# Kernel optimization log

Hardware: AMD Instinct MI355X
Metric: run time of the kernel (lower is better)

## Reference

```python
import jax, jax.numpy as jnp
import numpy as np

B, C, N, T = 8, 256, 768, 12
HID = C // 4          # divided_hidden=4 -> hidden=64
HEADS = 1
D = HID // HEADS      # head_dim = 64
SCALE = D ** (-0.5)
EPS = 1e-6


def conv1x1(x, w, b):
    # x: [b,c,n,t], w: [o,c], b: [o]
    return jnp.einsum('bcnt,oc->bont', x, w) + b[:, None, None]


def layernorm_cf(x, w, b):
    # channels_first LayerNorm over axis 1
    u = x.mean(1, keepdims=True)
    s = ((x - u) ** 2).mean(1, keepdims=True)
    xh = (x - u) / jnp.sqrt(s + EPS)
    return w[:, None, None] * xh + b[:, None, None]


def setup_inputs() -> dict:
    key = jax.random.key(0)
    ks = jax.random.split(key, 32)
    f32 = jnp.float32
    inp = {
        'x': jax.random.normal(ks[0], (B, C, N, T), dtype=f32),
        'time_ind': jax.random.randint(ks[1], (B, T), 0, 288),
        'weekin': jax.random.randint(ks[2], (B, T), 0, 7),
        'holiin': jax.random.randint(ks[3], (B, T), 0, 2),
        'adj_s': jax.random.uniform(ks[4], (B, T, N, N), dtype=f32),
        'ln1_w': jnp.ones((C,), f32), 'ln1_b': jnp.zeros((C,), f32),
        'ln2_w': jnp.ones((C,), f32), 'ln2_b': jnp.zeros((C,), f32),
        'Wnq': jax.random.normal(ks[5], (C, HID), f32) * 0.05, 'bnq': jnp.zeros((HID,), f32),
        'Wnk': jax.random.normal(ks[6], (C, HID), f32) * 0.05, 'bnk': jnp.zeros((HID,), f32),
        'Wtq': jax.random.normal(ks[7], (C, HID), f32) * 0.05, 'btq': jnp.zeros((HID,), f32),
        'Wtk': jax.random.normal(ks[8], (C, HID), f32) * 0.05, 'btk': jnp.zeros((HID,), f32),
        'Bn': jax.random.normal(ks[9], (1, HEADS, N, N), f32) * 0.02,
        'Bt': jax.random.normal(ks[10], (1, HEADS, T, T), f32) * 0.02,
        'v_w': jax.random.normal(ks[11], (HID, C), f32) * 0.05, 'v_b': jnp.zeros((HID,), f32),
        'fcv_w': jax.random.normal(ks[12], (2 * HID, C), f32) * 0.05, 'fcv_b': jnp.zeros((2 * HID,), f32),
        'proj_w': jax.random.normal(ks[13], (C, 2 * HID), f32) * 0.05, 'proj_b': jnp.zeros((C,), f32),
        'ffn_w1': jax.random.normal(ks[14], (4 * C, C), f32) * 0.03, 'ffn_b1': jnp.zeros((4 * C,), f32),
        'ffn_w2': jax.random.normal(ks[15], (C, 2 * C), f32) * 0.03, 'ffn_b2': jnp.zeros((C,), f32),
    }
    return inp


def dual_axis(x, adj_s, Wnq, bnq, Wnk, bnk, Wtq, btq, Wtk, btk, Bn, Bt,
              v_w, v_b, fcv_w, fcv_b, proj_w, proj_b):
    # x: [b,f,n,t]; heads==1 so head dim folds into hidden.
    # --- node-axis attention ---
    xn = x.transpose(0, 3, 2, 1)                      # [b,t,n,f]
    nq = xn @ Wnq + bnq                               # [b,t,n,hid]
    nk = xn @ Wnk + bnk
    attn_n = jnp.einsum('btid,btjd->btij', nq, nk) * SCALE + Bn[0, 0]
    attn_n = jax.nn.softmax(attn_n, axis=-1) * adj_s  # [b,t,n,n]
    # --- time-axis attention ---
    xt = x.transpose(0, 2, 3, 1)                      # [b,n,t,f]
    tq = xt @ Wtq + btq                               # [b,n,t,hid]
    tk = xt @ Wtk + btk
    attn_t = jnp.einsum('bnid,bnjd->bnij', tq, tk) * SCALE + Bt[0, 0]
    attn_t = jax.nn.softmax(attn_t, axis=-1)          # [b,n,t,t]
    # --- values + nconv_2 aggregation ---
    v1 = conv1x1(x, v_w, v_b)                         # [b,hid,n,t]
    # sg: out[b,c,w,l] = sum_v v1[b,c,v,l] * attn_n[b,l,v,w]
    hs = jnp.einsum('bcvl,blvw->bcwl', v1, attn_n)    # [b,hid,n,t]
    # tg on time axis: v1 transposed to [b,hid,t,n]
    xtv = v1.transpose(0, 1, 3, 2)                    # [b,hid,t,n]
    tx = jnp.einsum('bcvl,blvw->bcwl', xtv, attn_t)   # [b,hid,t,n]
    ht = tx.transpose(0, 1, 3, 2)                     # [b,hid,n,t]
    h = jnp.concatenate([ht, hs], axis=1)             # [b,2hid,n,t]
    v = conv1x1(x, fcv_w, fcv_b)                      # [b,2hid,n,t]
    return conv1x1(h * v, proj_w, proj_b)             # [b,C,n,t]


def feedforward(x, w1, b1, w2, b2):
    y = conv1x1(x, w1, b1)                            # [b,4C,n,t]
    a, g = jnp.split(y, 2, axis=1)                    # each [b,2C,n,t]
    y = a * jax.nn.gelu(g, approximate=False)
    return conv1x1(y, w2, b2)


def reference(x, time_ind, weekin, holiin, adj_s,
              ln1_w, ln1_b, ln2_w, ln2_b,
              Wnq, bnq, Wnk, bnk, Wtq, btq, Wtk, btk, Bn, Bt,
              v_w, v_b, fcv_w, fcv_b, proj_w, proj_b,
              ffn_w1, ffn_b1, ffn_w2, ffn_b2):
    x1 = layernorm_cf(x, ln1_w, ln1_b)
    x = dual_axis(x1, adj_s, Wnq, bnq, Wnk, bnk, Wtq, btq, Wtk, btk, Bn, Bt,
                  v_w, v_b, fcv_w, fcv_b, proj_w, proj_b) + x
    x2 = layernorm_cf(x, ln2_w, ln2_b)
    x = feedforward(x2, ffn_w1, ffn_b1, ffn_w2, ffn_b2) + x
    return x
```

## Files before the change

kernel.cpp:

```cpp
#include <hip/hip_runtime.h>
#include <cstddef>

typedef unsigned short u16;
typedef __attribute__((ext_vector_type(8))) short bf16x8;
typedef __attribute__((ext_vector_type(4))) float f32x4;

constexpr int nB = 8, nC = 256, nN = 768, nT = 12, nM = nN * nT, nH = 64;
constexpr float SCALE = 0.125f;
constexpr float LNEPS = 1e-6f;

__device__ inline u16 f2b(float f) {
    union { float f; unsigned u; } v; v.f = f;
    unsigned r = v.u + 0x7FFFu + ((v.u >> 16) & 1u);
    return (u16)(r >> 16);
}
__device__ inline float b2f(u16 h) {
    union { unsigned u; float f; } v; v.u = ((unsigned)h) << 16;
    return v.f;
}
__device__ inline uint2 packb4(float a, float b, float c, float d) {
    uint2 r;
    r.x = (unsigned)f2b(a) | ((unsigned)f2b(b) << 16);
    r.y = (unsigned)f2b(c) | ((unsigned)f2b(d) << 16);
    return r;
}
__device__ inline f32x4 mfma16(bf16x8 a, bf16x8 b, f32x4 c) {
    return __builtin_amdgcn_mfma_f32_16x16x32_bf16(a, b, c, 0, 0, 0);
}

__device__ inline void stage64(const u16* __restrict__ g, int ld, u16* lds, int tid) {
#pragma unroll
    for (int r = 0; r < 2; ++r) {
        int c = tid + r * 256;
        int row = c >> 3, kc = (c & 7) * 8;
        *(uint4*)&lds[row * 72 + kc] = *(const uint4*)&g[(size_t)row * ld + kc];
    }
}

__device__ inline void mfma_block(const u16* As, const u16* Bs, f32x4 acc[2][2],
                                  int wo, int wm, int quad, int r) {
#pragma unroll
    for (int ks = 0; ks < 64; ks += 32) {
        bf16x8 a0 = *(const bf16x8*)&As[(wo + r) * 72 + ks + quad * 8];
        bf16x8 a1 = *(const bf16x8*)&As[(wo + 16 + r) * 72 + ks + quad * 8];
        bf16x8 b0 = *(const bf16x8*)&Bs[(wm + r) * 72 + ks + quad * 8];
        bf16x8 b1 = *(const bf16x8*)&Bs[(wm + 16 + r) * 72 + ks + quad * 8];
        acc[0][0] = mfma16(a0, b0, acc[0][0]);
        acc[0][1] = mfma16(a0, b1, acc[0][1]);
        acc[1][0] = mfma16(a1, b0, acc[1][0]);
        acc[1][1] = mfma16(a1, b1, acc[1][1]);
    }
}

__global__ __launch_bounds__(256) void cvt_w(const float* __restrict__ Wnq,
                                             const float* __restrict__ Wnk,
                                             const float* __restrict__ Wtq,
                                             const float* __restrict__ Wtk,
                                             const float* __restrict__ vw,
                                             const float* __restrict__ fcvw,
                                             const float* __restrict__ projw,
                                             const float* __restrict__ w1,
                                             const float* __restrict__ w2,
                                             u16* __restrict__ WB) {
    int i = blockIdx.x * 256 + threadIdx.x;
    float v;
    if (i < 65536) {
        int seg = i >> 14, j = i & 16383;
        int o = j >> 8, k = j & 255;
        const float* src = seg == 0 ? Wnq : seg == 1 ? Wnk : seg == 2 ? Wtq : Wtk;
        v = src[k * 64 + o];
    } else if (i < 81920)  v = vw[i - 65536];
    else if (i < 114688)   v = fcvw[i - 81920];
    else if (i < 147456)   v = projw[i - 114688];
    else if (i < 409600)   v = w1[i - 147456];
    else                   v = w2[i - 409600];
    WB[i] = f2b(v);
}

__global__ __launch_bounds__(256) void zero_f(float* __restrict__ p) {
    p[blockIdx.x * 256 + threadIdx.x] = 0.f;
}

__global__ __launch_bounds__(256) void ln_cl(const float* __restrict__ X,
                                             const float* __restrict__ w,
                                             const float* __restrict__ bias,
                                             u16* __restrict__ Y) {
    int tid = threadIdx.x;
    int lane = tid & 63, cg = tid >> 6;
    int m0 = blockIdx.x * 64, b = blockIdx.y;
    size_t base = (size_t)b * nC * nM + m0 + lane;
    float s = 0.f, ss = 0.f;
#pragma unroll 4
    for (int k = 0; k < 64; ++k) {
        float v = X[base + (size_t)(cg * 64 + k) * nM];
        s += v; ss += v * v;
    }
    __shared__ float rs[4][64], rss[4][64], mu_s[64], rstd_s[64];
    __shared__ u16 Lo[64][264];
    rs[cg][lane] = s; rss[cg][lane] = ss;
    __syncthreads();
    if (tid < 64) {
        float t1 = rs[0][lane] + rs[1][lane] + rs[2][lane] + rs[3][lane];
        float t2 = rss[0][lane] + rss[1][lane] + rss[2][lane] + rss[3][lane];
        float mu = t1 * (1.f / nC);
        float var = t2 * (1.f / nC) - mu * mu;
        mu_s[lane] = mu;
        rstd_s[lane] = rsqrtf(var + LNEPS);
    }
    __syncthreads();
    float mu = mu_s[lane], rstd = rstd_s[lane];
#pragma unroll 8
    for (int k = 0; k < 64; k += 2) {
        int c = cg * 64 + k;
        float v0 = (X[base + (size_t)c * nM] - mu) * rstd * w[c] + bias[c];
        float v1 = (X[base + (size_t)(c + 1) * nM] - mu) * rstd * w[c + 1] + bias[c + 1];
        *(unsigned*)&Lo[lane][c] = (unsigned)f2b(v0) | ((unsigned)f2b(v1) << 16);
    }
    __syncthreads();
#pragma unroll
    for (int r = 0; r < 8; ++r) {
        int c = tid + r * 256;
        int mm = c >> 5, ch = (c & 31) * 8;
        *(uint4*)&Y[((size_t)b * nM + m0 + mm) * 256 + ch] = *(uint4*)&Lo[mm][ch];
    }
}

template <int COUT, int LAYOUT>
__global__ __launch_bounds__(256) void gemm_proj(const u16* __restrict__ X,
                                                 const u16* __restrict__ W,
                                                 const float* __restrict__ bias,
                                                 u16* __restrict__ OUT) {
    __shared__ u16 As[64 * 72], Bs[64 * 72];
    int tid = threadIdx.x;
    int m0 = blockIdx.x * 64, o0 = blockIdx.y * 64, b = blockIdx.z;
    int lane = tid & 63, wid = tid >> 6;
    int wo = (wid & 1) * 32, wm = (wid >> 1) * 32;
    int quad = lane >> 4, r = lane & 15;
    const u16* Ag = W + (size_t)o0 * 256;
    const u16* Bg = X + ((size_t)b * nM + m0) * 256;
    f32x4 acc[2][2] = {};
    for (int k0 = 0; k0 < 256; k0 += 64) {
        __syncthreads();
        stage64(Ag + k0, 256, As, tid);
        stage64(Bg + k0, 256, Bs, tid);
        __syncthreads();
        mfma_block(As, Bs, acc, wo, wm, quad, r);
    }
#pragma unroll
    for (int oi = 0; oi < 2; ++oi)
#pragma unroll
        for (int mj = 0; mj < 2; ++mj) {
            int o = o0 + wo + oi * 16 + quad * 4;
            int m = m0 + wm + mj * 16 + r;
            f32x4 a = acc[oi][mj];
            float v0 = a[0] + bias[o], v1 = a[1] + bias[o + 1];
            float v2 = a[2] + bias[o + 2], v3 = a[3] + bias[o + 3];
            if (LAYOUT == 1) {
                *(uint2*)&OUT[((size_t)b * nM + m) * COUT + o] = packb4(v0, v1, v2, v3);
            } else if (LAYOUT == 0) {
                int n = m / 12, t = m - n * 12;
                *(uint2*)&OUT[((size_t)(b * 12 + t) * nN + n) * COUT + o] =
                    packb4(v0, v1, v2, v3);
            } else {
                int n = m / 12, t = m - n * 12;
                size_t bt = (size_t)(b * 12 + t) * 64;
                OUT[(bt + o) * nN + n]     = f2b(v0);
                OUT[(bt + o + 1) * nN + n] = f2b(v1);
                OUT[(bt + o + 2) * nN + n] = f2b(v2);
                OUT[(bt + o + 3) * nN + n] = f2b(v3);
            }
        }
}

__global__ __launch_bounds__(256) void scores_k(const u16* __restrict__ NQ,
                                                const u16* __restrict__ NK,
                                                const float* __restrict__ Bn,
                                                u16* __restrict__ SE,
                                                float* __restrict__ rowsum) {
    __shared__ u16 As[64 * 72], Bs[64 * 72];
    __shared__ float lsum[64];
    int tid = threadIdx.x;
    int j0 = blockIdx.x * 64, i0 = blockIdx.y * 64, bt = blockIdx.z;
    if (tid < 64) lsum[tid] = 0.f;
    int lane = tid & 63, wid = tid >> 6;
    int wo = (wid & 1) * 32, wm = (wid >> 1) * 32;
    int quad = lane >> 4, r = lane & 15;
    const u16* Ag = NQ + ((size_t)bt * nN + i0) * 64;
    const u16* Bg = NK + ((size_t)bt * nN + j0) * 64;
    f32x4 acc[2][2] = {};
    __syncthreads();
    stage64(Ag, 64, As, tid);
    stage64(Bg, 64, Bs, tid);
    __syncthreads();
    mfma_block(As, Bs, acc, wo, wm, quad, r);
#pragma unroll
    for (int oi = 0; oi < 2; ++oi) {
        f32x4 rsm = {0.f, 0.f, 0.f, 0.f};
#pragma unroll
        for (int mj = 0; mj < 2; ++mj) {
            int i_ = i0 + wo + oi * 16 + quad * 4;
            int j_ = j0 + wm + mj * 16 + r;
#pragma unroll
            for (int rr = 0; rr < 4; ++rr) {
                float s = acc[oi][mj][rr] * SCALE + Bn[(size_t)(i_ + rr) * nN + j_];
                float e = expf(s);
                SE[((size_t)bt * nN + i_ + rr) * nN + j_] = f2b(e);
                rsm[rr] += e;
            }
        }
#pragma unroll
        for (int mask = 1; mask < 16; mask <<= 1) {
            rsm[0] += __shfl_xor(rsm[0], mask);
            rsm[1] += __shfl_xor(rsm[1], mask);
            rsm[2] += __shfl_xor(rsm[2], mask);
            rsm[3] += __shfl_xor(rsm[3], mask);
        }
        if (r == 0) {
#pragma unroll
            for (int rr = 0; rr < 4; ++rr)
                atomicAdd(&lsum[wo + oi * 16 + quad * 4 + rr], rsm[rr]);
        }
    }
    __syncthreads();
    if (tid < 64) atomicAdd(&rowsum[(size_t)bt * nN + i0 + tid], lsum[tid]);
}

__global__ __launch_bounds__(256) void attn_fin(const u16* __restrict__ SE,
                                                const float* __restrict__ adj,
                                                const float* __restrict__ rowsum,
                                                u16* __restrict__ AT2) {
    __shared__ u16 Ls[64 * 72];
    __shared__ float rinv[64];
    int tid = threadIdx.x;
    int w0 = blockIdx.x * 64, v0 = blockIdx.y * 64, bt = blockIdx.z;
    if (tid < 64) rinv[tid] = 1.f / rowsum[(size_t)bt * nN + v0 + tid];
    __syncthreads();
    {
        int v = tid >> 2, wc = (tid & 3) * 16;
        const u16* se = SE + ((size_t)bt * nN + v0 + v) * nN + w0 + wc;
        const float* ad = adj + ((size_t)bt * nN + v0 + v) * nN + w0 + wc;
        float ri = rinv[v];
        union { uint4 q; u16 s[8]; } p0, p1;
#pragma unroll
        for (int ii = 0; ii < 8; ++ii) p0.s[ii] = f2b(b2f(se[ii]) * ad[ii] * ri);
#pragma unroll
        for (int ii = 0; ii < 8; ++ii) p1.s[ii] = f2b(b2f(se[8 + ii]) * ad[8 + ii] * ri);
        *(uint4*)&Ls[v * 72 + wc] = p0.q;
        *(uint4*)&Ls[v * 72 + wc + 8] = p1.q;
    }
    __syncthreads();
    {
        int w = tid >> 2, vc = (tid & 3) * 16;
        union { uint4 q; u16 s[8]; } p0, p1;
#pragma unroll
        for (int ii = 0; ii < 8; ++ii) p0.s[ii] = Ls[(vc + ii) * 72 + w];
#pragma unroll
        for (int ii = 0; ii < 8; ++ii) p1.s[ii] = Ls[(vc + 8 + ii) * 72 + w];
        u16* op = AT2 + ((size_t)bt * nN + w0 + w) * nN + v0 + vc;
        *(uint4*)&op[0] = p0.q;
        *(uint4*)&op[8] = p1.q;
    }
}

__global__ __launch_bounds__(256) void node_agg_k(const u16* __restrict__ V1N,
                                                  const u16* __restrict__ AT2,
                                                  u16* __restrict__ HB) {
    __shared__ u16 As[64 * 72], Bs[64 * 72];
    int tid = threadIdx.x;
    int w0 = blockIdx.x * 64, bt = blockIdx.z;
    int b = bt / 12, l = bt - b * 12;
    int lane = tid & 63, wid = tid >> 6;
    int wo = (wid & 1) * 32, wm = (wid >> 1) * 32;
    int quad = lane >> 4, r = lane & 15;
    const u16* Ag = V1N + (size_t)bt * 64 * nN;
    const u16* Bg = AT2 + ((size_t)bt * nN + w0) * nN;
    f32x4 acc[2][2] = {};
    for (int k0 = 0; k0 < nN; k0 += 64) {
        __syncthreads();
        stage64(Ag + k0, nN, As, tid);
        stage64(Bg + k0, nN, Bs, tid);
        __syncthreads();
        mfma_block(As, Bs, acc, wo, wm, quad, r);
    }
#pragma unroll
    for (int oi = 0; oi < 2; ++oi)
#pragma unroll
        for (int mj = 0; mj < 2; ++mj) {
            int c = wo + oi * 16 + quad * 4;
            int w = w0 + wm + mj * 16 + r;
            f32x4 a = acc[oi][mj];
            *(uint2*)&HB[((size_t)b * nM + w * 12 + l) * 128 + 64 + c] =
                packb4(a[0], a[1], a[2], a[3]);
        }
}

__global__ __launch_bounds__(192) void time_attn(const u16* __restrict__ TQ,
                                                 const u16* __restrict__ TK,
                                                 const float* __restrict__ Bt,
                                                 float* __restrict__ AT) {
    int bn = blockIdx.x;
    __shared__ float tqs[nT * 64], tks[nT * 64], ss[nT * nT];
    __shared__ float inv_s[nT], max_s[nT];
    int tid = threadIdx.x;
    size_t base = (size_t)bn * nT * 64;
#pragma unroll
    for (int r = 0; r < 4; ++r) {
        int idx = tid + r * 192;
        tqs[idx] = b2f(TQ[base + idx]);
        tks[idx] = b2f(TK[base + idx]);
    }
    __syncthreads();
    if (tid < 144) {
        int i = tid / 12, j = tid % 12;
        float s = 0.f;
#pragma unroll
        for (int h = 0; h < 64; ++h) s += tqs[i * 64 + h] * tks[j * 64 + h];
        ss[tid] = s * SCALE + Bt[i * 12 + j];
    }
    __syncthreads();
    if (tid < 12) {
        float mx = -1e30f;
        for (int j = 0; j < 12; ++j) mx = fmaxf(mx, ss[tid * 12 + j]);
        float sm = 0.f;
        for (int j = 0; j < 12; ++j) sm += expf(ss[tid * 12 + j] - mx);
        max_s[tid] = mx; inv_s[tid] = 1.f / sm;
    }
    __syncthreads();
    if (tid < 144) {
        int i = tid / 12;
        AT[(size_t)bn * 144 + tid] = expf(ss[tid] - max_s[i]) * inv_s[i];
    }
}

__global__ __launch_bounds__(256) void time_agg_k(const u16* __restrict__ V1N,
                                                  const float* __restrict__ AT,
                                                  u16* __restrict__ HB) {
    int tid = threadIdx.x;
    int lane = tid & 63, cg = tid >> 6;
    int n = blockIdx.x * 64 + lane;
    int b = blockIdx.y;
    size_t bn = (size_t)b * nN + n;
#pragma unroll 2
    for (int cc = 0; cc < 16; ++cc) {
        int c = cg * 16 + cc;
        float acc[12] = {};
        for (int v = 0; v < 12; ++v) {
            float val = b2f(V1N[((size_t)(b * 12 + v) * 64 + c) * nN + n]);
            const float4* at4 = (const float4*)(AT + bn * 144 + v * 12);
            float4 a0 = at4[0], a1 = at4[1], a2 = at4[2];
            acc[0] += val * a0.x;  acc[1] += val * a0.y;
            acc[2] += val * a0.z;  acc[3] += val * a0.w;
            acc[4] += val * a1.x;  acc[5] += val * a1.y;
            acc[6] += val * a1.z;  acc[7] += val * a1.w;
            acc[8] += val * a2.x;  acc[9] += val * a2.y;
            acc[10] += val * a2.z; acc[11] += val * a2.w;
        }
#pragma unroll
        for (int t = 0; t < 12; ++t)
            HB[((size_t)b * nM + n * 12 + t) * 128 + c] = f2b(acc[t]);
    }
}

__global__ __launch_bounds__(256) void prodproj_k(const u16* __restrict__ HB,
                                                  const u16* __restrict__ VG,
                                                  const u16* __restrict__ W,
                                                  const float* __restrict__ bias,
                                                  const float* __restrict__ RES,
                                                  float* __restrict__ OUT) {
    __shared__ u16 As[64 * 72], Bs[64 * 72];
    int tid = threadIdx.x;
    int m0 = blockIdx.x * 64, o0 = blockIdx.y * 64, b = blockIdx.z;
    int lane = tid & 63, wid = tid >> 6;
    int wo = (wid & 1) * 32, wm = (wid >> 1) * 32;
    int quad = lane >> 4, r = lane & 15;
    f32x4 acc[2][2] = {};
    for (int k0 = 0; k0 < 128; k0 += 64) {
        __syncthreads();
        stage64(W + (size_t)o0 * 128 + k0, 128, As, tid);
#pragma unroll
        for (int rr = 0; rr < 2; ++rr) {
            int c = tid + rr * 256;
            int row = c >> 3, kc = (c & 7) * 8;
            size_t gi = ((size_t)b * nM + m0 + row) * 128 + k0 + kc;
            uint4 hv = *(const uint4*)&HB[gi];
            uint4 vv = *(const uint4*)&VG[gi];
            u16* hs = (u16*)&hv; u16* vs = (u16*)&vv;
            union { uint4 q; u16 s[8]; } ov;
#pragma unroll
            for (int q2 = 0; q2 < 8; ++q2) ov.s[q2] = f2b(b2f(hs[q2]) * b2f(vs[q2]));
            *(uint4*)&Bs[row * 72 + kc] = ov.q;
        }
        __syncthreads();
        mfma_block(As, Bs, acc, wo, wm, quad, r);
    }
#pragma unroll
    for (int oi = 0; oi < 2; ++oi)
#pragma unroll
        for (int mj = 0; mj < 2; ++mj) {
            int o = o0 + wo + oi * 16 + quad * 4;
            int m = m0 + wm + mj * 16 + r;
            f32x4 a = acc[oi][mj];
#pragma unroll
            for (int rr = 0; rr < 4; ++rr) {
                size_t idx = ((size_t)(b * nC + o + rr)) * nM + m;
                OUT[idx] = a[rr] + bias[o + rr] + RES[idx];
            }
        }
}

__global__ __launch_bounds__(256) void ffn1_k(const u16* __restrict__ X,
                                              const u16* __restrict__ W1,
                                              const float* __restrict__ B1,
                                              u16* __restrict__ G1) {
    __shared__ u16 As[64 * 72], Gs[64 * 72], Bs[64 * 72];
    int tid = threadIdx.x;
    int m0 = blockIdx.x * 64, o0 = blockIdx.y * 64, b = blockIdx.z;
    int lane = tid & 63, wid = tid >> 6;
    int wo = (wid & 1) * 32, wm = (wid >> 1) * 32;
    int quad = lane >> 4, r = lane & 15;
    f32x4 acca[2][2] = {}, accg[2][2] = {};
    for (int k0 = 0; k0 < 256; k0 += 64) {
        __syncthreads();
        stage64(W1 + (size_t)o0 * 256 + k0, 256, As, tid);
        stage64(W1 + (size_t)(512 + o0) * 256 + k0, 256, Gs, tid);
        stage64(X + ((size_t)b * nM + m0) * 256 + k0, 256, Bs, tid);
        __syncthreads();
#pragma unroll
        for (int ks = 0; ks < 64; ks += 32) {
            bf16x8 a0 = *(const bf16x8*)&As[(wo + r) * 72 + ks + quad * 8];
            bf16x8 a1 = *(const bf16x8*)&As[(wo + 16 + r) * 72 + ks + quad * 8];
            bf16x8 g0 = *(const bf16x8*)&Gs[(wo + r) * 72 + ks + quad * 8];
            bf16x8 g1 = *(const bf16x8*)&Gs[(wo + 16 + r) * 72 + ks + quad * 8];
            bf16x8 b0 = *(const bf16x8*)&Bs[(wm + r) * 72 + ks + quad * 8];
            bf16x8 b1 = *(const bf16x8*)&Bs[(wm + 16 + r) * 72 + ks + quad * 8];
            acca[0][0] = mfma16(a0, b0, acca[0][0]);
            acca[0][1] = mfma16(a0, b1, acca[0][1]);
            acca[1][0] = mfma16(a1, b0, acca[1][0]);
            acca[1][1] = mfma16(a1, b1, acca[1][1]);
            accg[0][0] = mfma16(g0, b0, accg[0][0]);
            accg[0][1] = mfma16(g0, b1, accg[0][1]);
            accg[1][0] = mfma16(g1, b0, accg[1][0]);
            accg[1][1] = mfma16(g1, b1, accg[1][1]);
        }
    }
#pragma unroll
    for (int oi = 0; oi < 2; ++oi)
#pragma unroll
        for (int mj = 0; mj < 2; ++mj) {
            int o = o0 + wo + oi * 16 + quad * 4;
            int m = m0 + wm + mj * 16 + r;
            float vals[4];
#pragma unroll
            for (int rr = 0; rr < 4; ++rr) {
                float aa = acca[oi][mj][rr] + B1[o + rr];
                float gg = accg[oi][mj][rr] + B1[512 + o + rr];
                float gl = 0.5f * gg * (1.f + erff(gg * 0.70710678118654752f));
                vals[rr] = aa * gl;
            }
            *(uint2*)&G1[((size_t)b * nM + m) * 512 + o] =
                packb4(vals[0], vals[1], vals[2], vals[3]);
        }
}

__global__ __launch_bounds__(256) void ffn2_k(const u16* __restrict__ G1,
                                              const u16* __restrict__ W2,
                                              const float* __restrict__ B2,
                                              const float* __restrict__ RES,
                                              float* __restrict__ OUT) {
    __shared__ u16 As[64 * 72], Bs[64 * 72];
    int tid = threadIdx.x;
    int m0 = blockIdx.x * 64, o0 = blockIdx.y * 64, b = blockIdx.z;
    int lane = tid & 63, wid = tid >> 6;
    int wo = (wid & 1) * 32, wm = (wid >> 1) * 32;
    int quad = lane >> 4, r = lane & 15;
    f32x4 acc[2][2] = {};
    for (int k0 = 0; k0 < 512; k0 += 64) {
        __syncthreads();
        stage64(W2 + (size_t)o0 * 512 + k0, 512, As, tid);
        stage64(G1 + ((size_t)b * nM + m0) * 512 + k0, 512, Bs, tid);
        __syncthreads();
        mfma_block(As, Bs, acc, wo, wm, quad, r);
    }
#pragma unroll
    for (int oi = 0; oi < 2; ++oi)
#pragma unroll
        for (int mj = 0; mj < 2; ++mj) {
            int o = o0 + wo + oi * 16 + quad * 4;
            int m = m0 + wm + mj * 16 + r;
            f32x4 a = acc[oi][mj];
#pragma unroll
            for (int rr = 0; rr < 4; ++rr) {
                size_t idx = ((size_t)(b * nC + o + rr)) * nM + m;
                OUT[idx] = a[rr] + B2[o + rr] + RES[idx];
            }
        }
}

extern "C" void kernel_launch(void* const* d_in, const int* in_sizes, int n_in,
                              void* d_out, int out_size, void* d_ws, size_t ws_size,
                              hipStream_t stream) {
    const float* x      = (const float*)d_in[0];
    const float* adj    = (const float*)d_in[4];
    const float* ln1w   = (const float*)d_in[5];
    const float* ln1b   = (const float*)d_in[6];
    const float* ln2w   = (const float*)d_in[7];
    const float* ln2b   = (const float*)d_in[8];
    const float* Wnq    = (const float*)d_in[9];
    const float* bnq    = (const float*)d_in[10];
    const float* Wnk    = (const float*)d_in[11];
    const float* bnk    = (const float*)d_in[12];
    const float* Wtq    = (const float*)d_in[13];
    const float* btq    = (const float*)d_in[14];
    const float* Wtk    = (const float*)d_in[15];
    const float* btk    = (const float*)d_in[16];
    const float* Bn     = (const float*)d_in[17];
    const float* Bt     = (const float*)d_in[18];
    const float* v_w    = (const float*)d_in[19];
    const float* v_b    = (const float*)d_in[20];
    const float* fcv_w  = (const float*)d_in[21];
    const float* fcv_b  = (const float*)d_in[22];
    const float* proj_w = (const float*)d_in[23];
    const float* proj_b = (const float*)d_in[24];
    const float* w1     = (const float*)d_in[25];
    const float* b1     = (const float*)d_in[26];
    const float* w2     = (const float*)d_in[27];
    const float* b2     = (const float*)d_in[28];
    float* out = (float*)d_out;

    char* p = (char*)d_ws;
    auto alloc = [&](size_t bytes) { char* q = p; p += (bytes + 255) & ~(size_t)255; return q; };
    u16*   x1cl   = (u16*)alloc(37748736);
    u16*   nqb    = (u16*)alloc(9437184);
    u16*   nkb    = (u16*)alloc(9437184);
    u16*   SE     = (u16*)alloc(113246208);
    u16*   AT2    = (u16*)alloc(113246208);
    u16*   v1n    = (u16*)alloc(9437184);
    float* atT    = (float*)alloc(3538944);
    u16*   hb     = (u16*)alloc(18874368);
    u16*   vg     = (u16*)alloc(18874368);
    float* rowsum = (float*)alloc(294912);
    u16*   WB     = (u16*)alloc(1081344);
    float* xr   = (float*)SE;
    u16*   x2cl = AT2;
    u16*   g1   = (u16*)((char*)AT2 + 37748736);

    dim3 blk(256);
    zero_f<<<dim3(288), blk, 0, stream>>>(rowsum);
    cvt_w<<<dim3(2112), blk, 0, stream>>>(Wnq, Wnk, Wtq, Wtk, v_w, fcv_w, proj_w,
                                          w1, w2, WB);
    ln_cl<<<dim3(144, nB), blk, 0, stream>>>(x, ln1w, ln1b, x1cl);
    gemm_proj<64, 0><<<dim3(144, 1, nB), blk, 0, stream>>>(x1cl, WB + 0, bnq, nqb);
    gemm_proj<64, 0><<<dim3(144, 1, nB), blk, 0, stream>>>(x1cl, WB + 16384, bnk, nkb);
    scores_k<<<dim3(12, 12, nB * nT), blk, 0, stream>>>(nqb, nkb, Bn, SE, rowsum);
    attn_fin<<<dim3(12, 12, nB * nT), blk, 0, stream>>>(SE, adj, rowsum, AT2);
    gemm_proj<64, 1><<<dim3(144, 1, nB), blk, 0, stream>>>(x1cl, WB + 32768, btq, nqb);
    gemm_proj<64, 1><<<dim3(144, 1, nB), blk, 0, stream>>>(x1cl, WB + 49152, btk, nkb);
    time_attn<<<dim3(nB * nN), dim3(192), 0, stream>>>(nqb, nkb, Bt, atT);
    gemm_proj<64, 2><<<dim3(144, 1, nB), blk, 0, stream>>>(x1cl, WB + 65536, v_b, v1n);
    node_agg_k<<<dim3(12, 1, nB * nT), blk, 0, stream>>>(v1n, AT2, hb);
    time_agg_k<<<dim3(12, nB), blk, 0, stream>>>(v1n, atT, hb);
    gemm_proj<128, 1><<<dim3(144, 2, nB), blk, 0, stream>>>(x1cl, WB + 81920, fcv_b, vg);
    prodproj_k<<<dim3(144, 4, nB), blk, 0, stream>>>(hb, vg, WB + 114688, proj_b, x, xr);
    ln_cl<<<dim3(144, nB), blk, 0, stream>>>(xr, ln2w, ln2b, x2cl);
    ffn1_k<<<dim3(144, 8, nB), blk, 0, stream>>>(x2cl, WB + 147456, b1, g1);
    ffn2_k<<<dim3(144, 4, nB), blk, 0, stream>>>(g1, WB + 409600, b2, xr, out);
}
```

Before: 983.2 us.

## Fuse attention finalize into node aggregation and retile projection/FFN GEMMs to 128

Removes the attn_fin kernel and its 113 MB AT2 intermediate by applying the adj multiply, row normalization and transpose while staging tiles inside the node aggregation GEMM. Merges the paired Q/K projections into one dual-output kernel that shares the X tile. Replaces the 64x64 projection, FFN1 and FFN2 GEMMs with 128-wide tiles so more work is done per loaded tile. The fused staging does scattered 2-byte shared-memory stores, which may cause bank conflicts, and it allocates a new SC buffer.

New measurement: 985.2 us. Within noise of the previous version (+0.2%).

```diff
diff --git a/kernel.cpp b/kernel.cpp
--- a/kernel.cpp
+++ b/kernel.cpp
@@ -6,6 +6,7 @@
 typedef __attribute__((ext_vector_type(4))) float f32x4;
 
 constexpr int nB = 8, nC = 256, nN = 768, nT = 12, nM = nN * nT, nH = 64;
+constexpr int nMtot = nB * nM;
 constexpr float SCALE = 0.125f;
 constexpr float LNEPS = 1e-6f;
 
@@ -125,18 +126,17 @@
     }
 }
 
-template <int COUT, int LAYOUT>
-__global__ __launch_bounds__(256) void gemm_proj(const u16* __restrict__ X,
-                                                 const u16* __restrict__ W,
-                                                 const float* __restrict__ bias,
-                                                 u16* __restrict__ OUT) {
+__global__ __launch_bounds__(256) void gemm_v1(const u16* __restrict__ X,
+                                               const u16* __restrict__ W,
+                                               const float* __restrict__ bias,
+                                               u16* __restrict__ OUT) {
     __shared__ u16 As[64 * 72], Bs[64 * 72];
     int tid = threadIdx.x;
-    int m0 = blockIdx.x * 64, o0 = blockIdx.y * 64, b = blockIdx.z;
+    int m0 = blockIdx.x * 64, b = blockIdx.y;
     int lane = tid & 63, wid = tid >> 6;
     int wo = (wid & 1) * 32, wm = (wid >> 1) * 32;
     int quad = lane >> 4, r = lane & 15;
-    const u16* Ag = W + (size_t)o0 * 256;
+    const u16* Ag = W;
     const u16* Bg = X + ((size_t)b * nM + m0) * 256;
     f32x4 acc[2][2] = {};
     for (int k0 = 0; k0 < 256; k0 += 64) {
@@ -150,24 +150,183 @@
     for (int oi = 0; oi < 2; ++oi)
 #pragma unroll
         for (int mj = 0; mj < 2; ++mj) {
-            int o = o0 + wo + oi * 16 + quad * 4;
+            int o = wo + oi * 16 + quad * 4;
             int m = m0 + wm + mj * 16 + r;
+            int n = m / 12, t = m - n * 12;
+            size_t bt = (size_t)(b * 12 + t) * 64;
             f32x4 a = acc[oi][mj];
-            float v0 = a[0] + bias[o], v1 = a[1] + bias[o + 1];
-            float v2 = a[2] + bias[o + 2], v3 = a[3] + bias[o + 3];
-            if (LAYOUT == 1) {
-                *(uint2*)&OUT[((size_t)b * nM + m) * COUT + o] = packb4(v0, v1, v2, v3);
-            } else if (LAYOUT == 0) {
-                int n = m / 12, t = m - n * 12;
-                *(uint2*)&OUT[((size_t)(b * 12 + t) * nN + n) * COUT + o] =
-                    packb4(v0, v1, v2, v3);
+            OUT[(bt + o) * nN + n]     = f2b(a[0] + bias[o]);
+            OUT[(bt + o + 1) * nN + n] = f2b(a[1] + bias[o + 1]);
+            OUT[(bt + o + 2) * nN + n] = f2b(a[2] + bias[o + 2]);
+            OUT[(bt + o + 3) * nN + n] = f2b(a[3] + bias[o + 3]);
+        }
+}
+
+template <int MODE>
+__global__ __launch_bounds__(256) void dual64(const u16* __restrict__ X,
+                                              const u16* __restrict__ Wa,
+                                              const u16* __restrict__ Wb,
+                                              const float* __restrict__ ba,
+                                              const float* __restrict__ bb,
+                                              u16* __restrict__ OA,
+                                              u16* __restrict__ OB,
+                                              int K) {
+    __shared__ u16 Was[64 * 72], Wbs[64 * 72], Xs[128 * 72];
+    int tid = threadIdx.x;
+    int m0 = blockIdx.x * 128, o0 = blockIdx.y * 64;
+    int lane = tid & 63, wid = tid >> 6;
+    int wo = (wid & 1) * 32, wm = (wid >> 1) * 64;
+    int quad = lane >> 4, r = lane & 15;
+    const u16* WaP = Wa + (size_t)o0 * K;
+    const u16* WbP = Wb + (size_t)o0 * K;
+    f32x4 accA[2][4] = {}, accB[2][4] = {};
+    for (int k0 = 0; k0 < K; k0 += 64) {
+        __syncthreads();
+#pragma unroll
+        for (int it = 0; it < 2; ++it) {
+            int idx = tid + it * 256;
+            int row = idx >> 3, c8 = (idx & 7) * 8;
+            *(uint4*)&Was[row * 72 + c8] = *(const uint4*)&WaP[(size_t)row * K + k0 + c8];
+            *(uint4*)&Wbs[row * 72 + c8] = *(const uint4*)&WbP[(size_t)row * K + k0 + c8];
+        }
+#pragma unroll
+        for (int it = 0; it < 4; ++it) {
+            int idx = tid + it * 256;
+            int row = idx >> 3, c8 = (idx & 7) * 8;
+            *(uint4*)&Xs[row * 72 + c8] = *(const uint4*)&X[(size_t)(m0 + row) * K + k0 + c8];
+        }
+        __syncthreads();
+#pragma unroll
+        for (int ks = 0; ks < 64; ks += 32) {
+            bf16x8 aA[2], aB[2], bx[4];
+#pragma unroll
+            for (int i = 0; i < 2; ++i) {
+                aA[i] = *(const bf16x8*)&Was[(wo + i * 16 + r) * 72 + ks + quad * 8];
+                aB[i] = *(const bf16x8*)&Wbs[(wo + i * 16 + r) * 72 + ks + quad * 8];
+            }
+#pragma unroll
+            for (int j = 0; j < 4; ++j)
+                bx[j] = *(const bf16x8*)&Xs[(wm + j * 16 + r) * 72 + ks + quad * 8];
+#pragma unroll
+            for (int i = 0; i < 2; ++i)
+#pragma unroll
+                for (int j = 0; j < 4; ++j) {
+                    accA[i][j] = mfma16(aA[i], bx[j], accA[i][j]);
+                    accB[i][j] = mfma16(aB[i], bx[j], accB[i][j]);
+                }
+        }
+    }
+#pragma unroll
+    for (int i = 0; i < 2; ++i)
+#pragma unroll
+        for (int j = 0; j < 4; ++j) {
+            int o = o0 + wo + i * 16 + quad * 4;
+            int m = m0 + wm + j * 16 + r;
+            f32x4 a = accA[i][j], g = accB[i][j];
+            if (MODE == 2) {
+                float vals[4];
+#pragma unroll
+                for (int rr = 0; rr < 4; ++rr) {
+                    float aa = a[rr] + ba[o + rr];
+                    float gg = g[rr] + bb[o + rr];
+                    float gl = 0.5f * gg * (1.f + erff(gg * 0.70710678118654752f));
+                    vals[rr] = aa * gl;
+                }
+                *(uint2*)&OA[(size_t)m * 512 + o] = packb4(vals[0], vals[1], vals[2], vals[3]);
             } else {
-                int n = m / 12, t = m - n * 12;
-                size_t bt = (size_t)(b * 12 + t) * 64;
-                OUT[(bt + o) * nN + n]     = f2b(v0);
-                OUT[(bt + o + 1) * nN + n] = f2b(v1);
-                OUT[(bt + o + 2) * nN + n] = f2b(v2);
-                OUT[(bt + o + 3) * nN + n] = f2b(v3);
+                size_t row;
+                if (MODE == 0) {
+                    int b = m / nM, mm = m - b * nM;
+                    int n = mm / 12, t = mm - n * 12;
+                    row = (size_t)(b * 12 + t) * nN + n;
+                } else {
+                    row = (size_t)m;
+                }
+                *(uint2*)&OA[row * 64 + o] =
+                    packb4(a[0] + ba[o], a[1] + ba[o + 1], a[2] + ba[o + 2], a[3] + ba[o + 3]);
+                *(uint2*)&OB[row * 64 + o] =
+                    packb4(g[0] + bb[o], g[1] + bb[o + 1], g[2] + bb[o + 2], g[3] + bb[o + 3]);
+            }
+        }
+}
+
+template <int EPI, bool PROD>
+__global__ __launch_bounds__(256) void gemm128(const u16* __restrict__ A,
+                                               const u16* __restrict__ B,
+                                               const u16* __restrict__ B2,
+                                               const float* __restrict__ bias,
+                                               const float* __restrict__ RES,
+                                               void* __restrict__ OUTv,
+                                               int K, int O) {
+    __shared__ u16 As[128 * 72], Bs[128 * 72];
+    int tid = threadIdx.x;
+    int m0 = blockIdx.x * 128, o0 = blockIdx.y * 128;
+    int lane = tid & 63, wid = tid >> 6;
+    int wo = (wid & 1) * 64, wm = (wid >> 1) * 64;
+    int quad = lane >> 4, r = lane & 15;
+    f32x4 acc[4][4] = {};
+    for (int k0 = 0; k0 < K; k0 += 64) {
+        __syncthreads();
+#pragma unroll
+        for (int it = 0; it < 4; ++it) {
+            int idx = tid + it * 256;
+            int row = idx >> 3, c8 = (idx & 7) * 8;
+            *(uint4*)&As[row * 72 + c8] = *(const uint4*)&A[(size_t)(o0 + row) * K + k0 + c8];
+        }
+#pragma unroll
+        for (int it = 0; it < 4; ++it) {
+            int idx = tid + it * 256;
+            int row = idx >> 3, c8 = (idx & 7) * 8;
+            size_t gi = (size_t)(m0 + row) * K + k0 + c8;
+            if (!PROD) {
+                *(uint4*)&Bs[row * 72 + c8] = *(const uint4*)&B[gi];
+            } else {
+                uint4 hv = *(const uint4*)&B[gi];
+                uint4 vv = *(const uint4*)&B2[gi];
+                u16* hs = (u16*)&hv; u16* vs = (u16*)&vv;
+                union { uint4 q; u16 s[8]; } ov;
+#pragma unroll
+                for (int q2 = 0; q2 < 8; ++q2) ov.s[q2] = f2b(b2f(hs[q2]) * b2f(vs[q2]));
+                *(uint4*)&Bs[row * 72 + c8] = ov.q;
+            }
+        }
+        __syncthreads();
+#pragma unroll
+        for (int ks = 0; ks < 64; ks += 32) {
+            bf16x8 av[4], bv[4];
+#pragma unroll
+            for (int i = 0; i < 4; ++i)
+                av[i] = *(const bf16x8*)&As[(wo + i * 16 + r) * 72 + ks + quad * 8];
+#pragma unroll
+            for (int j = 0; j < 4; ++j)
+                bv[j] = *(const bf16x8*)&Bs[(wm + j * 16 + r) * 72 + ks + quad * 8];
+#pragma unroll
+            for (int i = 0; i < 4; ++i)
+#pragma unroll
+                for (int j = 0; j < 4; ++j)
+                    acc[i][j] = mfma16(av[i], bv[j], acc[i][j]);
+        }
+    }
+#pragma unroll
+    for (int i = 0; i < 4; ++i)
+#pragma unroll
+        for (int j = 0; j < 4; ++j) {
+            int o = o0 + wo + i * 16 + quad * 4;
+            int m = m0 + wm + j * 16 + r;
+            f32x4 a = acc[i][j];
+            if (EPI == 0) {
+                u16* OUT = (u16*)OUTv;
+                *(uint2*)&OUT[(size_t)m * O + o] =
+                    packb4(a[0] + bias[o], a[1] + bias[o + 1],
+                           a[2] + bias[o + 2], a[3] + bias[o + 3]);
+            } else {
+                float* OUT = (float*)OUTv;
+                int b = m / nM, mm = m - b * nM;
+                size_t idx = ((size_t)b * O + o) * nM + mm;
+#pragma unroll
+                for (int rr = 0; rr < 4; ++rr)
+                    OUT[idx + (size_t)rr * nM] =
+                        a[rr] + bias[o + rr] + RES[idx + (size_t)rr * nM];
             }
         }
 }
@@ -225,60 +384,43 @@
     if (tid < 64) atomicAdd(&rowsum[(size_t)bt * nN + i0 + tid], lsum[tid]);
 }
 
-__global__ __launch_bounds__(256) void attn_fin(const u16* __restrict__ SE,
-                                                const float* __restrict__ adj,
-                                                const float* __restrict__ rowsum,
-                                                u16* __restrict__ AT2) {
-    __shared__ u16 Ls[64 * 72];
-    __shared__ float rinv[64];
-    int tid = threadIdx.x;
-    int w0 = blockIdx.x * 64, v0 = blockIdx.y * 64, bt = blockIdx.z;
-    if (tid < 64) rinv[tid] = 1.f / rowsum[(size_t)bt * nN + v0 + tid];
-    __syncthreads();
-    {
-        int v = tid >> 2, wc = (tid & 3) * 16;
-        const u16* se = SE + ((size_t)bt * nN + v0 + v) * nN + w0 + wc;
-        const float* ad = adj + ((size_t)bt * nN + v0 + v) * nN + w0 + wc;
-        float ri = rinv[v];
-        union { uint4 q; u16 s[8]; } p0, p1;
-#pragma unroll
-        for (int ii = 0; ii < 8; ++ii) p0.s[ii] = f2b(b2f(se[ii]) * ad[ii] * ri);
-#pragma unroll
-        for (int ii = 0; ii < 8; ++ii) p1.s[ii] = f2b(b2f(se[8 + ii]) * ad[8 + ii] * ri);
-        *(uint4*)&Ls[v * 72 + wc] = p0.q;
-        *(uint4*)&Ls[v * 72 + wc + 8] = p1.q;
-    }
-    __syncthreads();
-    {
-        int w = tid >> 2, vc = (tid & 3) * 16;
-        union { uint4 q; u16 s[8]; } p0, p1;
-#pragma unroll
-        for (int ii = 0; ii < 8; ++ii) p0.s[ii] = Ls[(vc + ii) * 72 + w];
-#pragma unroll
-        for (int ii = 0; ii < 8; ++ii) p1.s[ii] = Ls[(vc + 8 + ii) * 72 + w];
-        u16* op = AT2 + ((size_t)bt * nN + w0 + w) * nN + v0 + vc;
-        *(uint4*)&op[0] = p0.q;
-        *(uint4*)&op[8] = p1.q;
-    }
-}
-
-__global__ __launch_bounds__(256) void node_agg_k(const u16* __restrict__ V1N,
-                                                  const u16* __restrict__ AT2,
+__global__ __launch_bounds__(256) void node_agg_f(const u16* __restrict__ V1N,
+                                                  const u16* __restrict__ SE,
+                                                  const float* __restrict__ adj,
+                                                  const float* __restrict__ rowsum,
                                                   u16* __restrict__ HB) {
     __shared__ u16 As[64 * 72], Bs[64 * 72];
     int tid = threadIdx.x;
-    int w0 = blockIdx.x * 64, bt = blockIdx.z;
+    int w0 = blockIdx.x * 64, bt = blockIdx.y;
     int b = bt / 12, l = bt - b * 12;
     int lane = tid & 63, wid = tid >> 6;
     int wo = (wid & 1) * 32, wm = (wid >> 1) * 32;
     int quad = lane >> 4, r = lane & 15;
     const u16* Ag = V1N + (size_t)bt * 64 * nN;
-    const u16* Bg = AT2 + ((size_t)bt * nN + w0) * nN;
+    int v = tid >> 2, wc = (tid & 3) * 16;
     f32x4 acc[2][2] = {};
-    for (int k0 = 0; k0 < nN; k0 += 64) {
-        __syncthreads();
-        stage64(Ag + k0, nN, As, tid);
-        stage64(Bg + k0, nN, Bs, tid);
+    for (int v0 = 0; v0 < nN; v0 += 64) {
+        __syncthreads();
+        stage64(Ag + v0, nN, As, tid);
+        {
+            size_t rowg = (size_t)bt * nN + v0 + v;
+            float ri = 1.f / rowsum[rowg];
+            const u16* se = SE + rowg * nN + w0 + wc;
+            const float* ad = adj + rowg * nN + w0 + wc;
+            uint4 s0 = *(const uint4*)&se[0], s1 = *(const uint4*)&se[8];
+            float4 a0 = *(const float4*)&ad[0], a1 = *(const float4*)&ad[4];
+            float4 a2 = *(const float4*)&ad[8], a3 = *(const float4*)&ad[12];
+            const u16* sp0 = (const u16*)&s0;
+            const u16* sp1 = (const u16*)&s1;
+            float av[16] = {a0.x, a0.y, a0.z, a0.w, a1.x, a1.y, a1.z, a1.w,
+                            a2.x, a2.y, a2.z, a2.w, a3.x, a3.y, a3.z, a3.w};
+#pragma unroll
+            for (int ii = 0; ii < 8; ++ii)
+                Bs[(wc + ii) * 72 + v] = f2b(b2f(sp0[ii]) * av[ii] * ri);
+#pragma unroll
+            for (int ii = 0; ii < 8; ++ii)
+                Bs[(wc + 8 + ii) * 72 + v] = f2b(b2f(sp1[ii]) * av[8 + ii] * ri);
+        }
         __syncthreads();
         mfma_block(As, Bs, acc, wo, wm, quad, r);
     }
@@ -359,141 +501,6 @@
         for (int t = 0; t < 12; ++t)
             HB[((size_t)b * nM + n * 12 + t) * 128 + c] = f2b(acc[t]);
     }
-}
-
-__global__ __launch_bounds__(256) void prodproj_k(const u16* __restrict__ HB,
-                                                  const u16* __restrict__ VG,
-                                                  const u16* __restrict__ W,
-                                                  const float* __restrict__ bias,
-                                                  const float* __restrict__ RES,
-                                                  float* __restrict__ OUT) {
-    __shared__ u16 As[64 * 72], Bs[64 * 72];
-    int tid = threadIdx.x;
-    int m0 = blockIdx.x * 64, o0 = blockIdx.y * 64, b = blockIdx.z;
-    int lane = tid & 63, wid = tid >> 6;
-    int wo = (wid & 1) * 32, wm = (wid >> 1) * 32;
-    int quad = lane >> 4, r = lane & 15;
-    f32x4 acc[2][2] = {};
-    for (int k0 = 0; k0 < 128; k0 += 64) {
-        __syncthreads();
-        stage64(W + (size_t)o0 * 128 + k0, 128, As, tid);
-#pragma unroll
-        for (int rr = 0; rr < 2; ++rr) {
-            int c = tid + rr * 256;
-            int row = c >> 3, kc = (c & 7) * 8;
-            size_t gi = ((size_t)b * nM + m0 + row) * 128 + k0 + kc;
-            uint4 hv = *(const uint4*)&HB[gi];
-            uint4 vv = *(const uint4*)&VG[gi];
-            u16* hs = (u16*)&hv; u16* vs = (u16*)&vv;
-            union { uint4 q; u16 s[8]; } ov;
-#pragma unroll
-            for (int q2 = 0; q2 < 8; ++q2) ov.s[q2] = f2b(b2f(hs[q2]) * b2f(vs[q2]));
-            *(uint4*)&Bs[row * 72 + kc] = ov.q;
-        }
-        __syncthreads();
-        mfma_block(As, Bs, acc, wo, wm, quad, r);
-    }
-#pragma unroll
-    for (int oi = 0; oi < 2; ++oi)
-#pragma unroll
-        for (int mj = 0; mj < 2; ++mj) {
-            int o = o0 + wo + oi * 16 + quad * 4;
-            int m = m0 + wm + mj * 16 + r;
-            f32x4 a = acc[oi][mj];
-#pragma unroll
-            for (int rr = 0; rr < 4; ++rr) {
-                size_t idx = ((size_t)(b * nC + o + rr)) * nM + m;
-                OUT[idx] = a[rr] + bias[o + rr] + RES[idx];
-            }
-        }
-}
-
-__global__ __launch_bounds__(256) void ffn1_k(const u16* __restrict__ X,
-                                              const u16* __restrict__ W1,
-                                              const float* __restrict__ B1,
-                                              u16* __restrict__ G1) {
-    __shared__ u16 As[64 * 72], Gs[64 * 72], Bs[64 * 72];
-    int tid = threadIdx.x;
-    int m0 = blockIdx.x * 64, o0 = blockIdx.y * 64, b = blockIdx.z;
-    int lane = tid & 63, wid = tid >> 6;
-    int wo = (wid & 1) * 32, wm = (wid >> 1) * 32;
-    int quad = lane >> 4, r = lane & 15;
-    f32x4 acca[2][2] = {}, accg[2][2] = {};
-    for (int k0 = 0; k0 < 256; k0 += 64) {
-        __syncthreads();
-        stage64(W1 + (size_t)o0 * 256 + k0, 256, As, tid);
-        stage64(W1 + (size_t)(512 + o0) * 256 + k0, 256, Gs, tid);
-        stage64(X + ((size_t)b * nM + m0) * 256 + k0, 256, Bs, tid);
-        __syncthreads();
-#pragma unroll
-        for (int ks = 0; ks < 64; ks += 32) {
-            bf16x8 a0 = *(const bf16x8*)&As[(wo + r) * 72 + ks + quad * 8];
-            bf16x8 a1 = *(const bf16x8*)&As[(wo + 16 + r) * 72 + ks + quad * 8];
-            bf16x8 g0 = *(const bf16x8*)&Gs[(wo + r) * 72 + ks + quad * 8];
-            bf16x8 g1 = *(const bf16x8*)&Gs[(wo + 16 + r) * 72 + ks + quad * 8];
-            bf16x8 b0 = *(const bf16x8*)&Bs[(wm + r) * 72 + ks + quad * 8];
-            bf16x8 b1 = *(const bf16x8*)&Bs[(wm + 16 + r) * 72 + ks + quad * 8];
-            acca[0][0] = mfma16(a0, b0, acca[0][0]);
-            acca[0][1] = mfma16(a0, b1, acca[0][1]);
-            acca[1][0] = mfma16(a1, b0, acca[1][0]);
-            acca[1][1] = mfma16(a1, b1, acca[1][1]);
-            accg[0][0] = mfma16(g0, b0, accg[0][0]);
-            accg[0][1] = mfma16(g0, b1, accg[0][1]);
-            accg[1][0] = mfma16(g1, b0, accg[1][0]);
-            accg[1][1] = mfma16(g1, b1, accg[1][1]);
-        }
-    }
-#pragma unroll
-    for (int oi = 0; oi < 2; ++oi)
-#pragma unroll
-        for (int mj = 0; mj < 2; ++mj) {
-            int o = o0 + wo + oi * 16 + quad * 4;
-            int m = m0 + wm + mj * 16 + r;
-            float vals[4];
-#pragma unroll
-            for (int rr = 0; rr < 4; ++rr) {
-                float aa = acca[oi][mj][rr] + B1[o + rr];
-                float gg = accg[oi][mj][rr] + B1[512 + o + rr];
-                float gl = 0.5f * gg * (1.f + erff(gg * 0.70710678118654752f));
-                vals[rr] = aa * gl;
-            }
-            *(uint2*)&G1[((size_t)b * nM + m) * 512 + o] =
-                packb4(vals[0], vals[1], vals[2], vals[3]);
-        }
-}
-
-__global__ __launch_bounds__(256) void ffn2_k(const u16* __restrict__ G1,
-                                              const u16* __restrict__ W2,
-                                              const float* __restrict__ B2,
-                                              const float* __restrict__ RES,
-                                              float* __restrict__ OUT) {
-    __shared__ u16 As[64 * 72], Bs[64 * 72];
-    int tid = threadIdx.x;
-    int m0 = blockIdx.x * 64, o0 = blockIdx.y * 64, b = blockIdx.z;
-    int lane = tid & 63, wid = tid >> 6;
-    int wo = (wid & 1) * 32, wm = (wid >> 1) * 32;
-    int quad = lane >> 4, r = lane & 15;
-    f32x4 acc[2][2] = {};
-    for (int k0 = 0; k0 < 512; k0 += 64) {
-        __syncthreads();
-        stage64(W2 + (size_t)o0 * 512 + k0, 512, As, tid);
-        stage64(G1 + ((size_t)b * nM + m0) * 512 + k0, 512, Bs, tid);
-        __syncthreads();
-        mfma_block(As, Bs, acc, wo, wm, quad, r);
-    }
-#pragma unroll
-    for (int oi = 0; oi < 2; ++oi)
-#pragma unroll
-        for (int mj = 0; mj < 2; ++mj) {
-            int o = o0 + wo + oi * 16 + quad * 4;
-            int m = m0 + wm + mj * 16 + r;
-            f32x4 a = acc[oi][mj];
-#pragma unroll
-            for (int rr = 0; rr < 4; ++rr) {
-                size_t idx = ((size_t)(b * nC + o + rr)) * nM + m;
-                OUT[idx] = a[rr] + B2[o + rr] + RES[idx];
-            }
-        }
 }
 
 extern "C" void kernel_launch(void* const* d_in, const int* in_sizes, int n_in,
@@ -533,35 +540,38 @@
     u16*   nqb    = (u16*)alloc(9437184);
     u16*   nkb    = (u16*)alloc(9437184);
     u16*   SE     = (u16*)alloc(113246208);
-    u16*   AT2    = (u16*)alloc(113246208);
+    float* SC     = (float*)alloc(75497472);
     u16*   v1n    = (u16*)alloc(9437184);
     float* atT    = (float*)alloc(3538944);
     u16*   hb     = (u16*)alloc(18874368);
     u16*   vg     = (u16*)alloc(18874368);
     float* rowsum = (float*)alloc(294912);
     u16*   WB     = (u16*)alloc(1081344);
-    float* xr   = (float*)SE;
-    u16*   x2cl = AT2;
-    u16*   g1   = (u16*)((char*)AT2 + 37748736);
+    float* xr   = SC;
+    u16*   x2cl = SE;
+    u16*   g1   = (u16*)((char*)SE + 37748736);
 
     dim3 blk(256);
     zero_f<<<dim3(288), blk, 0, stream>>>(rowsum);
     cvt_w<<<dim3(2112), blk, 0, stream>>>(Wnq, Wnk, Wtq, Wtk, v_w, fcv_w, proj_w,
                                           w1, w2, WB);
     ln_cl<<<dim3(144, nB), blk, 0, stream>>>(x, ln1w, ln1b, x1cl);
-    gemm_proj<64, 0><<<dim3(144, 1, nB), blk, 0, stream>>>(x1cl, WB + 0, bnq, nqb);
-    gemm_proj<64, 0><<<dim3(144, 1, nB), blk, 0, stream>>>(x1cl, WB + 16384, bnk, nkb);
+    dual64<0><<<dim3(576, 1), blk, 0, stream>>>(x1cl, WB + 0, WB + 16384,
+                                                bnq, bnk, nqb, nkb, 256);
     scores_k<<<dim3(12, 12, nB * nT), blk, 0, stream>>>(nqb, nkb, Bn, SE, rowsum);
-    attn_fin<<<dim3(12, 12, nB * nT), blk, 0, stream>>>(SE, adj, rowsum, AT2);
-    gemm_proj<64, 1><<<dim3(144, 1, nB), blk, 0, stream>>>(x1cl, WB + 32768, btq, nqb);
-    gemm_proj<64, 1><<<dim3(144, 1, nB), blk, 0, stream>>>(x1cl, WB + 49152, btk, nkb);
+    dual64<1><<<dim3(576, 1), blk, 0, stream>>>(x1cl, WB + 32768, WB + 49152,
+                                                btq, btk, nqb, nkb, 256);
     time_attn<<<dim3(nB * nN), dim3(192), 0, stream>>>(nqb, nkb, Bt, atT);
-    gemm_proj<64, 2><<<dim3(144, 1, nB), blk, 0, stream>>>(x1cl, WB + 65536, v_b, v1n);
-    node_agg_k<<<dim3(12, 1, nB * nT), blk, 0, stream>>>(v1n, AT2, hb);
+    gemm_v1<<<dim3(144, nB), blk, 0, stream>>>(x1cl, WB + 65536, v_b, v1n);
+    node_agg_f<<<dim3(12, nB * nT), blk, 0, stream>>>(v1n, SE, adj, rowsum, hb);
     time_agg_k<<<dim3(12, nB), blk, 0, stream>>>(v1n, atT, hb);
-    gemm_proj<128, 1><<<dim3(144, 2, nB), blk, 0, stream>>>(x1cl, WB + 81920, fcv_b, vg);
-    prodproj_k<<<dim3(144, 4, nB), blk, 0, stream>>>(hb, vg, WB + 114688, proj_b, x, xr);
+    gemm128<0, false><<<dim3(576, 1), blk, 0, stream>>>(WB + 81920, x1cl, nullptr,
+                                                        fcv_b, nullptr, vg, 256, 128);
+    gemm128<1, true><<<dim3(576, 2), blk, 0, stream>>>(WB + 114688, hb, vg,
+                                                       proj_b, x, xr, 128, 256);
     ln_cl<<<dim3(144, nB), blk, 0, stream>>>(xr, ln2w, ln2b, x2cl);
-    ffn1_k<<<dim3(144, 8, nB), blk, 0, stream>>>(x2cl, WB + 147456, b1, g1);
-    ffn2_k<<<dim3(144, 4, nB), blk, 0, stream>>>(g1, WB + 409600, b2, xr, out);
-}
+    dual64<2><<<dim3(576, 8), blk, 0, stream>>>(x2cl, WB + 147456, WB + 147456 + 512 * 256,
+                                                b1, b1 + 512, g1, nullptr, 256);
+    gemm128<1, false><<<dim3(576, 2), blk, 0, stream>>>(WB + 409600, g1, nullptr,
+                                                        b2, xr, out, 512, 256);
+}
```
